# Kernel optimization log

Measured on AMD Instinct MI355X. Metric: run time of the kernel, lower is better.

## Reference

```python
import jax, jax.numpy as jnp
import numpy as np

TAU = 0.5

def setup_inputs() -> dict:
    key = jax.random.key(0)
    ks = jax.random.split(key, 8)
    B_Nq, B_Ns, C, H, W = 16, 16, 512, 32, 32
    f_q = jax.random.normal(ks[0], (B_Nq, C, H, W), dtype=jnp.float32)
    f_s = jax.random.normal(ks[1], (B_Ns, C, H, W), dtype=jnp.float32)
    # depthwise 1x1 convs with groups=dim, bias=False -> per-channel scalar weights [C]
    w_cca_q = jax.random.normal(ks[2], (C,), dtype=jnp.float32)
    w_cca_k = jax.random.normal(ks[3], (C,), dtype=jnp.float32)
    w_cca_v = jax.random.normal(ks[4], (C,), dtype=jnp.float32)
    w_sca_q = jax.random.normal(ks[5], (C,), dtype=jnp.float32)
    w_sca_k = jax.random.normal(ks[6], (C,), dtype=jnp.float32)
    lam = jnp.float32(0.1)
    return {"f_q": f_q, "f_s": f_s, "w_cca_q": w_cca_q, "w_cca_k": w_cca_k,
            "w_cca_v": w_cca_v, "w_sca_q": w_sca_q, "w_sca_k": w_sca_k, "lam": lam}

def _dw(x, w):
    # depthwise 1x1 conv, no bias == per-channel scale; x: [B,C,H,W], w: [C]
    return x * w[None, :, None, None]

def reference(f_q, f_s, w_cca_q, w_cca_k, w_cca_v, w_sca_q, w_sca_k, lam):
    B_Nq, C, H, W = f_q.shape
    B_Ns = f_s.shape[0]
    P = H * W
    qc = _dw(f_q, w_cca_q).reshape(B_Nq, C, P)          # [B,C,P]
    kc_mean = _dw(f_s, w_cca_k).reshape(B_Ns, C, P).mean(axis=0)  # [C,P]
    vc_mean = _dw(f_s, w_cca_v).reshape(B_Ns, C, P).mean(axis=0)  # [C,P]
    # channel attention: [B,C,C]
    Ac = jax.nn.softmax(jnp.einsum('bcp,dp->bcd', qc, kc_mean) / P, axis=-1)
    f_cca_q = jnp.einsum('bcd,dp->bcp', Ac, vc_mean).reshape(B_Nq, C, H, W)
    qs = _dw(f_cca_q, w_sca_q).reshape(B_Nq, C, P)      # [B,C,P]
    ks_mean = _dw(f_s, w_sca_k).reshape(B_Ns, C, P).mean(axis=0)  # [C,P]
    # spatial affinity: [B,P,P]
    M = jnp.einsum('bcp,cq->bpq', qs, ks_mean) / (TAU * C)
    alpha = jax.nn.softmax(M.mean(axis=-1), axis=-1)    # [B_Nq,P]
    beta = jax.nn.softmax(M.mean(axis=-2), axis=-1)     # [B_Nq,P]
    beta_mean = jnp.broadcast_to(beta.mean(axis=0, keepdims=True), (B_Ns, P))
    Fq_out = f_q + lam * f_cca_q
    return (Fq_out, alpha, beta_mean)
```

## Files before the change

### kernel.cpp

```cpp
#include <hip/hip_runtime.h>

typedef __bf16 bf16;
typedef __bf16 bf16x4 __attribute__((ext_vector_type(4)));
typedef __bf16 bf16x8 __attribute__((ext_vector_type(8)));
typedef float f32x4 __attribute__((ext_vector_type(4)));


#define GLL16(g, l)                                                             \
    __builtin_amdgcn_global_load_lds((const __attribute__((address_space(1))) void*)(g), \
                                     (__attribute__((address_space(3))) void*)(l), 16, 0, 0)

__device__ inline float wave_reduce_sum(float v) {
#pragma unroll
    for (int m = 32; m >= 1; m >>= 1) v += __shfl_xor(v, m, 64);
    return v;
}
__device__ inline float wave_reduce_max(float v) {
#pragma unroll
    for (int m = 32; m >= 1; m >>= 1) v = fmaxf(v, __shfl_xor(v, m, 64));
    return v;
}

__global__ void k_prep(const float* __restrict__ fs, const float* __restrict__ fq,
                       float* __restrict__ fsm32, bf16* __restrict__ fsm16,
                       bf16* __restrict__ fsmT, bf16* __restrict__ fq16) {
    __shared__ bf16 tile[32][33];
    int bx = blockIdx.x, by = blockIdx.y;
    int p0 = bx * 32, c0 = by * 32;
    int t = threadIdx.x;
    int cy = t >> 3, px = (t & 7) * 4;
    size_t off = (size_t)(c0 + cy) * 1024 + p0 + px;
    float4 s = {0.f, 0.f, 0.f, 0.f};
#pragma unroll
    for (int b = 0; b < 16; ++b) {
        float4 v = *(const float4*)(fs + (size_t)b * 524288 + off);
        s.x += v.x; s.y += v.y; s.z += v.z; s.w += v.w;
    }
    s.x *= (1.f / 16.f); s.y *= (1.f / 16.f); s.z *= (1.f / 16.f); s.w *= (1.f / 16.f);
    *(float4*)(fsm32 + off) = s;
    bf16x4 h4 = {(bf16)s.x, (bf16)s.y, (bf16)s.z, (bf16)s.w};
    *(bf16x4*)(fsm16 + off) = h4;
    tile[cy][px] = h4[0];
    tile[cy][px + 1] = h4[1];
    tile[cy][px + 2] = h4[2];
    tile[cy][px + 3] = h4[3];
    __syncthreads();
    int tx = t & 31, ty = t >> 5;
#pragma unroll
    for (int i = 0; i < 4; ++i)
        fsmT[(size_t)(p0 + ty + 8 * i) * 512 + c0 + tx] = tile[tx][ty + 8 * i];
    int blk = by * 32 + bx;
    const float4* f4 = (const float4*)fq;
#pragma unroll
    for (int i = 0; i < 16; ++i) {
        int idx = blk * 4096 + i * 256 + t;
        float4 v = f4[idx];
        bf16x4 q4 = {(bf16)v.x, (bf16)v.y, (bf16)v.z, (bf16)v.w};
        *(bf16x4*)(fq16 + (size_t)idx * 4) = q4;
    }
}

__global__ void k_u(const float* __restrict__ fsm32, const float* __restrict__ wsq,
                    const float* __restrict__ wsk, float* __restrict__ u,
                    float* __restrict__ rm) {
    int c = blockIdx.x;
    int t = threadIdx.x;
    float s = 0.f;
#pragma unroll
    for (int j = 0; j < 4; ++j) s += fsm32[(size_t)c * 1024 + t + 256 * j];
    s = wave_reduce_sum(s);
    __shared__ float red[4];
    int w = t >> 6, lane = t & 63;
    if (lane == 0) red[w] = s;
    __syncthreads();
    if (t == 0) {
        float rmv = (red[0] + red[1] + red[2] + red[3]) * (1.f / 1024.f);
        rm[c] = rmv;
        u[c] = wsq[c] * wsk[c] * rmv * (1.f / 256.f);
    }
}

__global__ void k_gemm1(const bf16* __restrict__ A, const bf16* __restrict__ B,
                        float* __restrict__ G) {
    __shared__ alignas(16) bf16 As[2][64 * 64];
    __shared__ alignas(16) bf16 Bs[2][128 * 64];
    const int dt = blockIdx.x, ct = blockIdx.y, b = blockIdx.z;
    const int t = threadIdx.x, w = t >> 6, lane = t & 63;
    const int quad = lane >> 4, r15 = lane & 15;
    const int wr = w & 1, wc = w >> 1;
    const bf16* Abase = A + ((size_t)(b * 512 + ct * 64)) * 1024;
    const bf16* Bbase = B + ((size_t)(dt * 128)) * 1024;
    const int srow = t >> 3, schunk = t & 7;
    f32x4 acc[2][4] = {};
    auto STAGE = [&](int buf, int k0) {
#pragma unroll
        for (int i = 0; i < 2; ++i) {
            int row = i * 32 + srow;
            int gchunk = schunk ^ (row & 7);
            GLL16(Abase + (size_t)row * 1024 + k0 + gchunk * 8, &As[buf][i * 2048 + t * 8]);
        }
#pragma unroll
        for (int i = 0; i < 4; ++i) {
            int row = i * 32 + srow;
            int gchunk = schunk ^ (row & 7);
            GLL16(Bbase + (size_t)row * 1024 + k0 + gchunk * 8, &Bs[buf][i * 2048 + t * 8]);
        }
    };
    STAGE(0, 0);
    __syncthreads();
    int cur = 0;
    for (int step = 0; step < 16; ++step) {
        if (step < 15) STAGE(cur ^ 1, (step + 1) * 64);
#pragma unroll
        for (int ks = 0; ks < 2; ++ks) {
            bf16x8 af[2], bfr[4];
#pragma unroll
            for (int mi = 0; mi < 2; ++mi) {
                int R = wr * 32 + mi * 16 + r15;
                int c = ks * 4 + quad;
                af[mi] = *(const bf16x8*)(&As[cur][R * 64 + ((c ^ (R & 7)) * 8)]);
            }
#pragma unroll
            for (int j = 0; j < 4; ++j) {
                int R = wc * 64 + j * 16 + r15;
                int c = ks * 4 + quad;
                bfr[j] = *(const bf16x8*)(&Bs[cur][R * 64 + ((c ^ (R & 7)) * 8)]);
            }
#pragma unroll
            for (int mi = 0; mi < 2; ++mi)
#pragma unroll
                for (int j = 0; j < 4; ++j)
                    acc[mi][j] = __builtin_amdgcn_mfma_f32_16x16x32_bf16(af[mi], bfr[j], acc[mi][j], 0, 0, 0);
        }
        __syncthreads();
        cur ^= 1;
    }
#pragma unroll
    for (int mi = 0; mi < 2; ++mi) {
        float* g = G + ((size_t)(b * 512 + ct * 64 + wr * 32 + mi * 16 + quad * 4)) * 512 +
                   dt * 128 + wc * 64 + r15;
#pragma unroll
        for (int j = 0; j < 4; ++j)
#pragma unroll
            for (int ii = 0; ii < 4; ++ii)
                g[(size_t)ii * 512 + j * 16] = acc[mi][j][ii];
    }
}

__global__ void k_softmax_ac(const float* __restrict__ G, const float* __restrict__ wq,
                             const float* __restrict__ wk, const float* __restrict__ wv,
                             const float* __restrict__ rm, bf16* __restrict__ Acw,
                             float* __restrict__ r, float* __restrict__ zbuf) {
    if (blockIdx.x < 128) zbuf[blockIdx.x * 256 + threadIdx.x] = 0.f;
    int row = blockIdx.x * 4 + (threadIdx.x >> 6);
    int lane = threadIdx.x & 63;
    int c = row & 511;
    const float* g = G + (size_t)row * 512;
    float sc = wq[c] * (1.f / 1024.f);
    float v[8];
    float mx = -3.4e38f;
#pragma unroll
    for (int j = 0; j < 8; ++j) {
        int d = lane + 64 * j;
        v[j] = g[d] * sc * wk[d];
        mx = fmaxf(mx, v[j]);
    }
    mx = wave_reduce_max(mx);
    float sum = 0.f;
#pragma unroll
    for (int j = 0; j < 8; ++j) {
        v[j] = __expf(v[j] - mx);
        sum += v[j];
    }
    sum = wave_reduce_sum(sum);
    float inv = 1.f / sum;
    bf16* o = Acw + (size_t)row * 512;
    float rsum = 0.f;
#pragma unroll
    for (int j = 0; j < 8; ++j) {
        int d = lane + 64 * j;
        float aw = v[j] * inv * wv[d];
        o[d] = (bf16)aw;
        rsum += aw * rm[d];
    }
    rsum = wave_reduce_sum(rsum);
    if (lane == 0) r[row] = rsum;
}

__global__ void k_gemm2(const bf16* __restrict__ A, const bf16* __restrict__ B,
                        const float* __restrict__ fq, const float* __restrict__ lamp,
                        const float* __restrict__ u, float* __restrict__ out,
                        float* __restrict__ alog) {
    __shared__ alignas(16) bf16 As[2][64 * 64];
    __shared__ alignas(16) bf16 Bs[2][128 * 64];
    const int pt = blockIdx.x, ct = blockIdx.y, b = blockIdx.z;
    const int t = threadIdx.x, w = t >> 6, lane = t & 63;
    const int quad = lane >> 4, r15 = lane & 15;
    const int wr = w & 1, wc = w >> 1;
    const bf16* Abase = A + ((size_t)(b * 512 + ct * 64)) * 512;
    const bf16* Bbase = B + ((size_t)(pt * 128)) * 512;
    const int srow = t >> 3, schunk = t & 7;
    f32x4 acc[2][4] = {};
    auto STAGE = [&](int buf, int k0) {
#pragma unroll
        for (int i = 0; i < 2; ++i) {
            int row = i * 32 + srow;
            int gchunk = schunk ^ (row & 7);
            GLL16(Abase + (size_t)row * 512 + k0 + gchunk * 8, &As[buf][i * 2048 + t * 8]);
        }
#pragma unroll
        for (int i = 0; i < 4; ++i) {
            int row = i * 32 + srow;
            int gchunk = schunk ^ (row & 7);
            GLL16(Bbase + (size_t)row * 512 + k0 + gchunk * 8, &Bs[buf][i * 2048 + t * 8]);
        }
    };
    STAGE(0, 0);
    __syncthreads();
    int cur = 0;
    for (int step = 0; step < 8; ++step) {
        if (step < 7) STAGE(cur ^ 1, (step + 1) * 64);
#pragma unroll
        for (int ks = 0; ks < 2; ++ks) {
            bf16x8 af[2], bfr[4];
#pragma unroll
            for (int mi = 0; mi < 2; ++mi) {
                int R = wr * 32 + mi * 16 + r15;
                int c = ks * 4 + quad;
                af[mi] = *(const bf16x8*)(&As[cur][R * 64 + ((c ^ (R & 7)) * 8)]);
            }
#pragma unroll
            for (int j = 0; j < 4; ++j) {
                int R = wc * 64 + j * 16 + r15;
                int c = ks * 4 + quad;
                bfr[j] = *(const bf16x8*)(&Bs[cur][R * 64 + ((c ^ (R & 7)) * 8)]);
            }
#pragma unroll
            for (int mi = 0; mi < 2; ++mi)
#pragma unroll
                for (int j = 0; j < 4; ++j)
                    acc[mi][j] = __builtin_amdgcn_mfma_f32_16x16x32_bf16(af[mi], bfr[j], acc[mi][j], 0, 0, 0);
        }
        __syncthreads();
        cur ^= 1;
    }
    float lam = lamp[0];
#pragma unroll
    for (int mi = 0; mi < 2; ++mi) {
        size_t rowbase = (size_t)(b * 512 + ct * 64 + wr * 32 + mi * 16 + quad * 4);
#pragma unroll
        for (int j = 0; j < 4; ++j)
#pragma unroll
            for (int ii = 0; ii < 4; ++ii) {
                size_t idx = (rowbase + ii) * 1024 + pt * 128 + wc * 64 + j * 16 + r15;
                out[idx] = fq[idx] + lam * acc[mi][j][ii];
            }
    }
    float uv[2][4];
#pragma unroll
    for (int mi = 0; mi < 2; ++mi)
#pragma unroll
        for (int ii = 0; ii < 4; ++ii)
            uv[mi][ii] = u[ct * 64 + wr * 32 + mi * 16 + quad * 4 + ii];
#pragma unroll
    for (int j = 0; j < 4; ++j) {
        float pv = 0.f;
#pragma unroll
        for (int mi = 0; mi < 2; ++mi)
#pragma unroll
            for (int ii = 0; ii < 4; ++ii)
                pv += uv[mi][ii] * acc[mi][j][ii];
        pv += __shfl_xor(pv, 16, 64);
        pv += __shfl_xor(pv, 32, 64);
        if (lane < 16)
            atomicAdd(alog + (size_t)b * 1024 + pt * 128 + wc * 64 + j * 16 + r15, pv);
    }
}

__global__ void k_blog(const float* __restrict__ r, const float* __restrict__ wsq,
                       const float* __restrict__ wsk, const float* __restrict__ fsm32,
                       float* __restrict__ blog) {
    int pq = blockIdx.x * 256 + threadIdx.x;
    int b = blockIdx.y;
    int c0 = blockIdx.z * 128;
    const float* rb = r + b * 512;
    float s0 = 0.f, s1 = 0.f, s2 = 0.f, s3 = 0.f;
#pragma unroll 4
    for (int c = c0; c < c0 + 128; c += 4) {
        s0 += rb[c] * wsq[c] * wsk[c] * fsm32[(size_t)c * 1024 + pq];
        s1 += rb[c + 1] * wsq[c + 1] * wsk[c + 1] * fsm32[(size_t)(c + 1) * 1024 + pq];
        s2 += rb[c + 2] * wsq[c + 2] * wsk[c + 2] * fsm32[(size_t)(c + 2) * 1024 + pq];
        s3 += rb[c + 3] * wsq[c + 3] * wsk[c + 3] * fsm32[(size_t)(c + 3) * 1024 + pq];
    }
    atomicAdd(&blog[(size_t)b * 1024 + pq], ((s0 + s1) + (s2 + s3)) * (1.f / 256.f));
}

__global__ void k_softmax_rows(const float* __restrict__ alog, const float* __restrict__ blog,
                               float* __restrict__ alpha_out, float* __restrict__ beta) {
    int z = blockIdx.x;
    int t = threadIdx.x;
    int w = t >> 6, lane = t & 63;
    const float* src = (z < 16) ? (alog + (size_t)z * 1024) : (blog + (size_t)(z - 16) * 1024);
    float v[4];
    float mx = -3.4e38f;
#pragma unroll
    for (int j = 0; j < 4; ++j) {
        v[j] = src[t + 256 * j];
        mx = fmaxf(mx, v[j]);
    }
    __shared__ float red[4];
    float wm = wave_reduce_max(mx);
    if (lane == 0) red[w] = wm;
    __syncthreads();
    mx = fmaxf(fmaxf(red[0], red[1]), fmaxf(red[2], red[3]));
    float s = 0.f;
#pragma unroll
    for (int j = 0; j < 4; ++j) {
        v[j] = __expf(v[j] - mx);
        s += v[j];
    }
    __syncthreads();
    float ws_ = wave_reduce_sum(s);
    if (lane == 0) red[w] = ws_;
    __syncthreads();
    s = red[0] + red[1] + red[2] + red[3];
    float inv = 1.f / s;
    if (z < 16) {
#pragma unroll
        for (int j = 0; j < 4; ++j) alpha_out[(size_t)z * 1024 + t + 256 * j] = v[j] * inv;
    } else {
#pragma unroll
        for (int j = 0; j < 4; ++j) beta[(size_t)(z - 16) * 1024 + t + 256 * j] = v[j] * inv;
    }
}

__global__ void k_betamean(const float* __restrict__ beta, float* __restrict__ out) {
    int q = blockIdx.x * 256 + threadIdx.x;
    float s = 0.f;
#pragma unroll
    for (int b = 0; b < 16; ++b) s += beta[b * 1024 + q];
    float val = s * (1.f / 16.f);
#pragma unroll
    for (int si = 0; si < 16; ++si) out[(size_t)si * 1024 + q] = val;
}

extern "C" void kernel_launch(void* const* d_in, const int* in_sizes, int n_in,
                              void* d_out, int out_size, void* d_ws, size_t ws_size,
                              hipStream_t stream) {
    const float* f_q = (const float*)d_in[0];
    const float* f_s = (const float*)d_in[1];
    const float* w_cca_q = (const float*)d_in[2];
    const float* w_cca_k = (const float*)d_in[3];
    const float* w_cca_v = (const float*)d_in[4];
    const float* w_sca_q = (const float*)d_in[5];
    const float* w_sca_k = (const float*)d_in[6];
    const float* lamp = (const float*)d_in[7];

    char* ws = (char*)d_ws;
    float* fsm32 = (float*)(ws + 0);
    bf16* fsm16 = (bf16*)(ws + 2097152);
    bf16* fsmT = (bf16*)(ws + 3145728);
    float* G = (float*)(ws + 4194304);
    bf16* Acw = (bf16*)(ws + 20971520);
    bf16* fq16 = (bf16*)(ws + 29360128);
    float* rm = (float*)(ws + 46137344);
    float* u = (float*)(ws + 46139392);
    float* r = (float*)(ws + 46141440);
    float* alog = (float*)(ws + 46239744);
    float* blog = (float*)(ws + 46305280);
    float* beta = (float*)(ws + 46370816);

    float* out_fq = (float*)d_out;
    float* out_alpha = out_fq + 8388608;
    float* out_bmean = out_fq + 8404992;

    k_prep<<<dim3(32, 16), 256, 0, stream>>>(f_s, f_q, fsm32, fsm16, fsmT, fq16);
    k_u<<<512, 256, 0, stream>>>(fsm32, w_sca_q, w_sca_k, u, rm);
    k_gemm1<<<dim3(4, 8, 16), 256, 0, stream>>>(fq16, fsm16, G);
    k_softmax_ac<<<2048, 256, 0, stream>>>(G, w_cca_q, w_cca_k, w_cca_v, rm, Acw, r, alog);
    k_gemm2<<<dim3(8, 8, 16), 256, 0, stream>>>(Acw, fsmT, f_q, lamp, u, out_fq, alog);
    k_blog<<<dim3(4, 16, 4), 256, 0, stream>>>(r, w_sca_q, w_sca_k, fsm32, blog);
    k_softmax_rows<<<32, 256, 0, stream>>>(alog, blog, out_alpha, beta);
    k_betamean<<<4, 256, 0, stream>>>(beta, out_bmean);
}
```

Baseline: 181.8 us.

## Fuse f_q bf16 conversion into gemm1 and deepen GEMM prefetch pipelining

Removes the separate f_q to bf16 pass from k_prep. gemm1 now streams fp32 f_q tiles directly into LDS with a 16-chunk XOR swizzle and converts them to bf16 at fragment load time. That avoids writing and re-reading a 16MB bf16 copy. Both GEMMs also switch to a two-stage-ahead prefetch using explicit vmcnt waits and raw barriers instead of __syncthreads. The fp32 A tile doubles gemm1's LDS footprint (which may lower occupancy) and adds conversion ALU work inside the MFMA loop.

```diff
diff --git a/kernel.cpp b/kernel.cpp
--- a/kernel.cpp
+++ b/kernel.cpp
@@ -21,9 +21,8 @@
     return v;
 }
 
-__global__ void k_prep(const float* __restrict__ fs, const float* __restrict__ fq,
-                       float* __restrict__ fsm32, bf16* __restrict__ fsm16,
-                       bf16* __restrict__ fsmT, bf16* __restrict__ fq16) {
+__global__ void k_prep(const float* __restrict__ fs, float* __restrict__ fsm32,
+                       bf16* __restrict__ fsm16, bf16* __restrict__ fsmT) {
     __shared__ bf16 tile[32][33];
     int bx = blockIdx.x, by = blockIdx.y;
     int p0 = bx * 32, c0 = by * 32;
@@ -49,15 +48,6 @@
 #pragma unroll
     for (int i = 0; i < 4; ++i)
         fsmT[(size_t)(p0 + ty + 8 * i) * 512 + c0 + tx] = tile[tx][ty + 8 * i];
-    int blk = by * 32 + bx;
-    const float4* f4 = (const float4*)fq;
-#pragma unroll
-    for (int i = 0; i < 16; ++i) {
-        int idx = blk * 4096 + i * 256 + t;
-        float4 v = f4[idx];
-        bf16x4 q4 = {(bf16)v.x, (bf16)v.y, (bf16)v.z, (bf16)v.w};
-        *(bf16x4*)(fq16 + (size_t)idx * 4) = q4;
-    }
 }
 
 __global__ void k_u(const float* __restrict__ fsm32, const float* __restrict__ wsq,
@@ -80,51 +70,54 @@
     }
 }
 
-__global__ void k_gemm1(const bf16* __restrict__ A, const bf16* __restrict__ B,
+__global__ void k_gemm1(const float* __restrict__ A, const bf16* __restrict__ B,
                         float* __restrict__ G) {
-    __shared__ alignas(16) bf16 As[2][64 * 64];
+    __shared__ alignas(16) float Asf[2][64 * 64];
     __shared__ alignas(16) bf16 Bs[2][128 * 64];
     const int dt = blockIdx.x, ct = blockIdx.y, b = blockIdx.z;
     const int t = threadIdx.x, w = t >> 6, lane = t & 63;
     const int quad = lane >> 4, r15 = lane & 15;
     const int wr = w & 1, wc = w >> 1;
-    const bf16* Abase = A + ((size_t)(b * 512 + ct * 64)) * 1024;
+    const float* Abase = A + ((size_t)(b * 512 + ct * 64)) * 1024;
     const bf16* Bbase = B + ((size_t)(dt * 128)) * 1024;
-    const int srow = t >> 3, schunk = t & 7;
     f32x4 acc[2][4] = {};
     auto STAGE = [&](int buf, int k0) {
 #pragma unroll
-        for (int i = 0; i < 2; ++i) {
-            int row = i * 32 + srow;
-            int gchunk = schunk ^ (row & 7);
-            GLL16(Abase + (size_t)row * 1024 + k0 + gchunk * 8, &As[buf][i * 2048 + t * 8]);
-        }
-#pragma unroll
         for (int i = 0; i < 4; ++i) {
-            int row = i * 32 + srow;
-            int gchunk = schunk ^ (row & 7);
-            GLL16(Bbase + (size_t)row * 1024 + k0 + gchunk * 8, &Bs[buf][i * 2048 + t * 8]);
+            int row = i * 16 + (t >> 4);
+            int gchunk = (t & 15) ^ (row & 15);
+            GLL16(Abase + (size_t)row * 1024 + k0 + gchunk * 4, &Asf[buf][(i * 256 + t) * 4]);
+        }
+#pragma unroll
+        for (int i = 0; i < 4; ++i) {
+            int row = i * 32 + (t >> 3);
+            int gchunk = (t & 7) ^ (row & 7);
+            GLL16(Bbase + (size_t)row * 1024 + k0 + gchunk * 8, &Bs[buf][(i * 256 + t) * 8]);
         }
     };
     STAGE(0, 0);
-    __syncthreads();
-    int cur = 0;
-    for (int step = 0; step < 16; ++step) {
-        if (step < 15) STAGE(cur ^ 1, (step + 1) * 64);
+    STAGE(1, 64);
+    for (int s = 0; s < 16; ++s) {
+        if (s < 15) asm volatile("s_waitcnt vmcnt(8)" ::: "memory");
+        else        asm volatile("s_waitcnt vmcnt(0)" ::: "memory");
+        __builtin_amdgcn_s_barrier();
+        const int cur = s & 1;
 #pragma unroll
         for (int ks = 0; ks < 2; ++ks) {
             bf16x8 af[2], bfr[4];
+            const int c8 = ks * 4 + quad;
 #pragma unroll
             for (int mi = 0; mi < 2; ++mi) {
                 int R = wr * 32 + mi * 16 + r15;
-                int c = ks * 4 + quad;
-                af[mi] = *(const bf16x8*)(&As[cur][R * 64 + ((c ^ (R & 7)) * 8)]);
+                f32x4 a0 = *(const f32x4*)(&Asf[cur][R * 64 + (((2 * c8) ^ (R & 15)) * 4)]);
+                f32x4 a1 = *(const f32x4*)(&Asf[cur][R * 64 + (((2 * c8 + 1) ^ (R & 15)) * 4)]);
+                af[mi] = bf16x8{(bf16)a0[0], (bf16)a0[1], (bf16)a0[2], (bf16)a0[3],
+                                (bf16)a1[0], (bf16)a1[1], (bf16)a1[2], (bf16)a1[3]};
             }
 #pragma unroll
             for (int j = 0; j < 4; ++j) {
                 int R = wc * 64 + j * 16 + r15;
-                int c = ks * 4 + quad;
-                bfr[j] = *(const bf16x8*)(&Bs[cur][R * 64 + ((c ^ (R & 7)) * 8)]);
+                bfr[j] = *(const bf16x8*)(&Bs[cur][R * 64 + ((c8 ^ (R & 7)) * 8)]);
             }
 #pragma unroll
             for (int mi = 0; mi < 2; ++mi)
@@ -132,8 +125,8 @@
                 for (int j = 0; j < 4; ++j)
                     acc[mi][j] = __builtin_amdgcn_mfma_f32_16x16x32_bf16(af[mi], bfr[j], acc[mi][j], 0, 0, 0);
         }
-        __syncthreads();
-        cur ^= 1;
+        __builtin_amdgcn_s_barrier();
+        if (s + 2 < 16) STAGE(cur, (s + 2) * 64);
     }
 #pragma unroll
     for (int mi = 0; mi < 2; ++mi) {
@@ -199,41 +192,41 @@
     const int wr = w & 1, wc = w >> 1;
     const bf16* Abase = A + ((size_t)(b * 512 + ct * 64)) * 512;
     const bf16* Bbase = B + ((size_t)(pt * 128)) * 512;
-    const int srow = t >> 3, schunk = t & 7;
     f32x4 acc[2][4] = {};
     auto STAGE = [&](int buf, int k0) {
 #pragma unroll
         for (int i = 0; i < 2; ++i) {
-            int row = i * 32 + srow;
-            int gchunk = schunk ^ (row & 7);
-            GLL16(Abase + (size_t)row * 512 + k0 + gchunk * 8, &As[buf][i * 2048 + t * 8]);
+            int row = i * 32 + (t >> 3);
+            int gchunk = (t & 7) ^ (row & 7);
+            GLL16(Abase + (size_t)row * 512 + k0 + gchunk * 8, &As[buf][(i * 256 + t) * 8]);
         }
 #pragma unroll
         for (int i = 0; i < 4; ++i) {
-            int row = i * 32 + srow;
-            int gchunk = schunk ^ (row & 7);
-            GLL16(Bbase + (size_t)row * 512 + k0 + gchunk * 8, &Bs[buf][i * 2048 + t * 8]);
+            int row = i * 32 + (t >> 3);
+            int gchunk = (t & 7) ^ (row & 7);
+            GLL16(Bbase + (size_t)row * 512 + k0 + gchunk * 8, &Bs[buf][(i * 256 + t) * 8]);
         }
     };
     STAGE(0, 0);
-    __syncthreads();
-    int cur = 0;
-    for (int step = 0; step < 8; ++step) {
-        if (step < 7) STAGE(cur ^ 1, (step + 1) * 64);
+    STAGE(1, 64);
+    for (int s = 0; s < 8; ++s) {
+        if (s < 7) asm volatile("s_waitcnt vmcnt(6)" ::: "memory");
+        else       asm volatile("s_waitcnt vmcnt(0)" ::: "memory");
+        __builtin_amdgcn_s_barrier();
+        const int cur = s & 1;
 #pragma unroll
         for (int ks = 0; ks < 2; ++ks) {
             bf16x8 af[2], bfr[4];
+            const int c8 = ks * 4 + quad;
 #pragma unroll
             for (int mi = 0; mi < 2; ++mi) {
                 int R = wr * 32 + mi * 16 + r15;
-                int c = ks * 4 + quad;
-                af[mi] = *(const bf16x8*)(&As[cur][R * 64 + ((c ^ (R & 7)) * 8)]);
+                af[mi] = *(const bf16x8*)(&As[cur][R * 64 + ((c8 ^ (R & 7)) * 8)]);
             }
 #pragma unroll
             for (int j = 0; j < 4; ++j) {
                 int R = wc * 64 + j * 16 + r15;
-                int c = ks * 4 + quad;
-                bfr[j] = *(const bf16x8*)(&Bs[cur][R * 64 + ((c ^ (R & 7)) * 8)]);
+                bfr[j] = *(const bf16x8*)(&Bs[cur][R * 64 + ((c8 ^ (R & 7)) * 8)]);
             }
 #pragma unroll
             for (int mi = 0; mi < 2; ++mi)
@@ -241,8 +234,8 @@
                 for (int j = 0; j < 4; ++j)
                     acc[mi][j] = __builtin_amdgcn_mfma_f32_16x16x32_bf16(af[mi], bfr[j], acc[mi][j], 0, 0, 0);
         }
-        __syncthreads();
-        cur ^= 1;
+        __builtin_amdgcn_s_barrier();
+        if (s + 2 < 8) STAGE(cur, (s + 2) * 64);
     }
     float lam = lamp[0];
 #pragma unroll
@@ -362,7 +355,6 @@
     bf16* fsmT = (bf16*)(ws + 3145728);
     float* G = (float*)(ws + 4194304);
     bf16* Acw = (bf16*)(ws + 20971520);
-    bf16* fq16 = (bf16*)(ws + 29360128);
     float* rm = (float*)(ws + 46137344);
     float* u = (float*)(ws + 46139392);
     float* r = (float*)(ws + 46141440);
@@ -374,9 +366,9 @@
     float* out_alpha = out_fq + 8388608;
     float* out_bmean = out_fq + 8404992;
 
-    k_prep<<<dim3(32, 16), 256, 0, stream>>>(f_s, f_q, fsm32, fsm16, fsmT, fq16);
+    k_prep<<<dim3(32, 16), 256, 0, stream>>>(f_s, fsm32, fsm16, fsmT);
     k_u<<<512, 256, 0, stream>>>(fsm32, w_sca_q, w_sca_k, u, rm);
-    k_gemm1<<<dim3(4, 8, 16), 256, 0, stream>>>(fq16, fsm16, G);
+    k_gemm1<<<dim3(4, 8, 16), 256, 0, stream>>>(f_q, fsm16, G);
     k_softmax_ac<<<2048, 256, 0, stream>>>(G, w_cca_q, w_cca_k, w_cca_v, rm, Acw, r, alog);
     k_gemm2<<<dim3(8, 8, 16), 256, 0, stream>>>(Acw, fsmT, f_q, lamp, u, out_fq, alog);
     k_blog<<<dim3(4, 16, 4), 256, 0, stream>>>(r, w_sca_q, w_sca_k, fsm32, blog);
```

After: 185.9 us. 2.3% more time.
